# Kernel optimization log

Hardware: AMD Instinct MI355X
Metric: run time of the kernel (lower is better)

## Reference

```python
import jax, jax.numpy as jnp
import numpy as np

HOPS = 3  # max_hops; C has HOPS+1 embedding tables


def setup_inputs() -> dict:
    key = jax.random.key(0)
    k1, k2 = jax.random.split(key)
    # story: [memory_len, batch, token_size]
    story = jax.random.randint(k1, (2048, 64, 4), 0, 50000, dtype=jnp.int64)
    # stacked embedding tables C_0..C_3: [hop+1, vocab, embed_dim], N(0, 0.1)
    C = 0.1 * jax.random.normal(k2, (HOPS + 1, 50000, 128), dtype=jnp.float32)
    return {"story": story, "C": C}


def reference(story, C):
    # story: [M, B, T] -> [B, M, T]
    story = jnp.transpose(story, (1, 0, 2))
    B, M, T = story.shape
    D = C.shape[-1]
    # padding_idx=0 semantics: embedding of token 0 is zero (fwd and bwd)
    pad_mask = (story != 0).astype(C.dtype)[..., None]  # [B, M, T, 1]

    u = jnp.zeros((B, D), dtype=C.dtype)
    for hop in range(HOPS):
        # gather + mask + sum over token dim -> memory keys m_A: [B, M, D]
        m_A = jnp.sum(C[hop][story] * pad_mask, axis=2)
        # attention scores over memory slots, softmax along M
        prob = jax.nn.softmax(jnp.einsum('bmd,bd->bm', m_A, u), axis=1)
        # memory values m_C from next-hop table: [B, M, D]
        m_C = jnp.sum(C[hop + 1][story] * pad_mask, axis=2)
        o_k = jnp.einsum('bm,bmd->bd', prob, m_C)
        u = u + o_k
    return u
```

## Files before the change

kernel.cpp:

```cpp
#include <hip/hip_runtime.h>

#define MM 2048
#define BB 64
#define TT 4
#define DD 128
#define VV 50000
#define VPAD 50176
#define NPART 392

typedef float f4v __attribute__((ext_vector_type(4)));
typedef short s8v __attribute__((ext_vector_type(8)));

__device__ __forceinline__ unsigned short f2bf(float f) {
    unsigned int u = __float_as_uint(f);
    u = u + 0x7FFFu + ((u >> 16) & 1u);
    return (unsigned short)(u >> 16);
}

__global__ void k_init(float4* __restrict__ p) {
    p[blockIdx.x * 256 + threadIdx.x] = make_float4(0.f, 0.f, 0.f, 0.f);
}

__global__ __launch_bounds__(256) void k_scatter0(const int* __restrict__ st,
                                                  float* __restrict__ W) {
    const int g = blockIdx.x * 256 + threadIdx.x;
    const int b = g & 63;
    const float p = 1.0f / (float)MM;
    const int4 tk = *(const int4*)(st + (size_t)g * 4);
    if (tk.x) atomicAdd(W + (size_t)tk.x * 64 + b, p);
    if (tk.y) atomicAdd(W + (size_t)tk.y * 64 + b, p);
    if (tk.z) atomicAdd(W + (size_t)tk.z * 64 + b, p);
    if (tk.w) atomicAdd(W + (size_t)tk.w * 64 + b, p);
}

__global__ __launch_bounds__(256, 3) void k_gemm_p(const float* __restrict__ Ch,
                                                   const float* __restrict__ u,
                                                   float* __restrict__ P) {
    __shared__ short lds[192 * 136];
    const int t = threadIdx.x;
    const int v0 = blockIdx.x * 128;

#pragma unroll
    for (int i = 0; i < 24; ++i) {
        const int G = i * 256 + t;
        const int row = G >> 5;
        const int c4 = G & 31;
        float4 val;
        if (row < 128) {
            const int v = v0 + row;
            val = (v < VV) ? *(const float4*)(Ch + (size_t)v * DD + c4 * 4)
                           : make_float4(0.f, 0.f, 0.f, 0.f);
        } else {
            val = *(const float4*)(u + (size_t)(row - 128) * DD + c4 * 4);
        }
        const unsigned int lo = ((unsigned int)f2bf(val.y) << 16) | f2bf(val.x);
        const unsigned int hi = ((unsigned int)f2bf(val.w) << 16) | f2bf(val.z);
        *(uint2*)(lds + row * 136 + c4 * 4) = make_uint2(lo, hi);
    }
    __syncthreads();

    const int l = t & 63;
    const int w = t >> 6;
    const int quad = l >> 4;
    const int n16 = l & 15;

    const int ar0 = (32 * w + n16) * 136;
    const int ar1 = (32 * w + 16 + n16) * 136;
    const int br0 = (128 + n16) * 136;
    const int br1 = (144 + n16) * 136;
    const int br2 = (160 + n16) * 136;
    const int br3 = (176 + n16) * 136;

    f4v c00 = {0.f, 0.f, 0.f, 0.f}, c01 = c00, c02 = c00, c03 = c00;
    f4v c10 = c00, c11 = c00, c12 = c00, c13 = c00;

#pragma unroll
    for (int s = 0; s < 4; ++s) {
        const int ko = s * 32 + quad * 8;
        const s8v a0 = *(const s8v*)(lds + ar0 + ko);
        const s8v a1 = *(const s8v*)(lds + ar1 + ko);
        const s8v b0 = *(const s8v*)(lds + br0 + ko);
        const s8v b1 = *(const s8v*)(lds + br1 + ko);
        const s8v b2 = *(const s8v*)(lds + br2 + ko);
        const s8v b3 = *(const s8v*)(lds + br3 + ko);
        c00 = __builtin_amdgcn_mfma_f32_16x16x32_bf16(a0, b0, c00, 0, 0, 0);
        c01 = __builtin_amdgcn_mfma_f32_16x16x32_bf16(a0, b1, c01, 0, 0, 0);
        c02 = __builtin_amdgcn_mfma_f32_16x16x32_bf16(a0, b2, c02, 0, 0, 0);
        c03 = __builtin_amdgcn_mfma_f32_16x16x32_bf16(a0, b3, c03, 0, 0, 0);
        c10 = __builtin_amdgcn_mfma_f32_16x16x32_bf16(a1, b0, c10, 0, 0, 0);
        c11 = __builtin_amdgcn_mfma_f32_16x16x32_bf16(a1, b1, c11, 0, 0, 0);
        c12 = __builtin_amdgcn_mfma_f32_16x16x32_bf16(a1, b2, c12, 0, 0, 0);
        c13 = __builtin_amdgcn_mfma_f32_16x16x32_bf16(a1, b3, c13, 0, 0, 0);
    }

    const int vb0 = v0 + 32 * w + quad * 4;
    const int vb1 = vb0 + 16;
#pragma unroll
    for (int r = 0; r < 4; ++r) {
        float* __restrict__ P0 = P + (size_t)(vb0 + r) * 64 + n16;
        P0[0] = c00[r]; P0[16] = c01[r]; P0[32] = c02[r]; P0[48] = c03[r];
        float* __restrict__ P1 = P + (size_t)(vb1 + r) * 64 + n16;
        P1[0] = c10[r]; P1[16] = c11[r]; P1[32] = c12[r]; P1[48] = c13[r];
    }
}

__global__ __launch_bounds__(512) void k_attn(const int* __restrict__ st,
                                              const float* __restrict__ P,
                                              float* __restrict__ W) {
    const int b = blockIdx.x;
    const int tid = threadIdx.x;
    __shared__ float redsum[8];

    const int4 tk0 = *(const int4*)(st + ((size_t)(tid + 0)    * 64 + b) * 4);
    const int4 tk1 = *(const int4*)(st + ((size_t)(tid + 512)  * 64 + b) * 4);
    const int4 tk2 = *(const int4*)(st + ((size_t)(tid + 1024) * 64 + b) * 4);
    const int4 tk3 = *(const int4*)(st + ((size_t)(tid + 1536) * 64 + b) * 4);

    float v0 = 0.f, v1 = 0.f, v2 = 0.f, v3 = 0.f;
    if (tk0.x) v0 += P[(size_t)tk0.x * 64 + b];
    if (tk0.y) v0 += P[(size_t)tk0.y * 64 + b];
    if (tk0.z) v0 += P[(size_t)tk0.z * 64 + b];
    if (tk0.w) v0 += P[(size_t)tk0.w * 64 + b];
    if (tk1.x) v1 += P[(size_t)tk1.x * 64 + b];
    if (tk1.y) v1 += P[(size_t)tk1.y * 64 + b];
    if (tk1.z) v1 += P[(size_t)tk1.z * 64 + b];
    if (tk1.w) v1 += P[(size_t)tk1.w * 64 + b];
    if (tk2.x) v2 += P[(size_t)tk2.x * 64 + b];
    if (tk2.y) v2 += P[(size_t)tk2.y * 64 + b];
    if (tk2.z) v2 += P[(size_t)tk2.z * 64 + b];
    if (tk2.w) v2 += P[(size_t)tk2.w * 64 + b];
    if (tk3.x) v3 += P[(size_t)tk3.x * 64 + b];
    if (tk3.y) v3 += P[(size_t)tk3.y * 64 + b];
    if (tk3.z) v3 += P[(size_t)tk3.z * 64 + b];
    if (tk3.w) v3 += P[(size_t)tk3.w * 64 + b];

    v0 = __expf(v0); v1 = __expf(v1); v2 = __expf(v2); v3 = __expf(v3);
    float sum = (v0 + v1) + (v2 + v3);
#pragma unroll
    for (int off = 32; off; off >>= 1) sum += __shfl_xor(sum, off, 64);
    if ((tid & 63) == 0) redsum[tid >> 6] = sum;
    __syncthreads();
    float tot = redsum[0];
#pragma unroll
    for (int i = 1; i < 8; ++i) tot += redsum[i];
    const float inv = 1.f / tot;

    v0 *= inv; v1 *= inv; v2 *= inv; v3 *= inv;

    if (tk0.x) atomicAdd(W + (size_t)tk0.x * 64 + b, v0);
    if (tk0.y) atomicAdd(W + (size_t)tk0.y * 64 + b, v0);
    if (tk0.z) atomicAdd(W + (size_t)tk0.z * 64 + b, v0);
    if (tk0.w) atomicAdd(W + (size_t)tk0.w * 64 + b, v0);
    if (tk1.x) atomicAdd(W + (size_t)tk1.x * 64 + b, v1);
    if (tk1.y) atomicAdd(W + (size_t)tk1.y * 64 + b, v1);
    if (tk1.z) atomicAdd(W + (size_t)tk1.z * 64 + b, v1);
    if (tk1.w) atomicAdd(W + (size_t)tk1.w * 64 + b, v1);
    if (tk2.x) atomicAdd(W + (size_t)tk2.x * 64 + b, v2);
    if (tk2.y) atomicAdd(W + (size_t)tk2.y * 64 + b, v2);
    if (tk2.z) atomicAdd(W + (size_t)tk2.z * 64 + b, v2);
    if (tk2.w) atomicAdd(W + (size_t)tk2.w * 64 + b, v2);
    if (tk3.x) atomicAdd(W + (size_t)tk3.x * 64 + b, v3);
    if (tk3.y) atomicAdd(W + (size_t)tk3.y * 64 + b, v3);
    if (tk3.z) atomicAdd(W + (size_t)tk3.z * 64 + b, v3);
    if (tk3.w) atomicAdd(W + (size_t)tk3.w * 64 + b, v3);
}

__global__ __launch_bounds__(256, 3) void k_gemm_o(const float* __restrict__ C2,
                                                   float* __restrict__ W,
                                                   float* __restrict__ upart,
                                                   const int rezero) {
    __shared__ unsigned Wt[64 * 68];
    __shared__ unsigned Ct[128 * 68];
    const int t = threadIdx.x;
    const int vb = blockIdx.x * 128;

#pragma unroll
    for (int i = 0; i < 4; ++i) {
        const int item = i * 256 + t;
        const int q = item & 15;
        const int p = item >> 4;
        float* w0 = W + (size_t)(vb + 2 * p) * 64 + 4 * q;
        float* w1 = W + (size_t)(vb + 2 * p + 1) * 64 + 4 * q;
        const float4 x = *(const float4*)w0;
        const float4 y = *(const float4*)w1;
        if (rezero) {
            *(float4*)w0 = make_float4(0.f, 0.f, 0.f, 0.f);
            *(float4*)w1 = make_float4(0.f, 0.f, 0.f, 0.f);
        }
        Wt[(4 * q + 0) * 68 + p] = ((unsigned)f2bf(y.x) << 16) | f2bf(x.x);
        Wt[(4 * q + 1) * 68 + p] = ((unsigned)f2bf(y.y) << 16) | f2bf(x.y);
        Wt[(4 * q + 2) * 68 + p] = ((unsigned)f2bf(y.z) << 16) | f2bf(x.z);
        Wt[(4 * q + 3) * 68 + p] = ((unsigned)f2bf(y.w) << 16) | f2bf(x.w);
    }
#pragma unroll
    for (int i = 0; i < 8; ++i) {
        const int item = i * 256 + t;
        const int q = item & 31;
        const int p = item >> 5;
        const int v0 = vb + 2 * p;
        const float4 x = (v0 < VV)
            ? *(const float4*)(C2 + (size_t)v0 * DD + 4 * q)
            : make_float4(0.f, 0.f, 0.f, 0.f);
        const float4 y = (v0 + 1 < VV)
            ? *(const float4*)(C2 + (size_t)(v0 + 1) * DD + 4 * q)
            : make_float4(0.f, 0.f, 0.f, 0.f);
        Ct[(4 * q + 0) * 68 + p] = ((unsigned)f2bf(y.x) << 16) | f2bf(x.x);
        Ct[(4 * q + 1) * 68 + p] = ((unsigned)f2bf(y.y) << 16) | f2bf(x.y);
        Ct[(4 * q + 2) * 68 + p] = ((unsigned)f2bf(y.z) << 16) | f2bf(x.z);
        Ct[(4 * q + 3) * 68 + p] = ((unsigned)f2bf(y.w) << 16) | f2bf(x.w);
    }
    __syncthreads();

    const int l = t & 63;
    const int w = t >> 6;
    const int quad = l >> 4;
    const int n16 = l & 15;

    f4v a00 = {0.f, 0.f, 0.f, 0.f}, a01 = a00;
    f4v a10 = a00, a11 = a00, a20 = a00, a21 = a00, a30 = a00, a31 = a00;

#pragma unroll
    for (int ch = 0; ch < 4; ++ch) {
        const int ku = ch * 16 + quad * 4;
        const s8v wa0 = *(const s8v*)&Wt[(0  + n16) * 68 + ku];
        const s8v wa1 = *(const s8v*)&Wt[(16 + n16) * 68 + ku];
        const s8v wa2 = *(const s8v*)&Wt[(32 + n16) * 68 + ku];
        const s8v wa3 = *(const s8v*)&Wt[(48 + n16) * 68 + ku];
        const s8v cb0 = *(const s8v*)&Ct[(w * 32 + n16) * 68 + ku];
        const s8v cb1 = *(const s8v*)&Ct[(w * 32 + 16 + n16) * 68 + ku];
        a00 = __builtin_amdgcn_mfma_f32_16x16x32_bf16(wa0, cb0, a00, 0, 0, 0);
        a01 = __builtin_amdgcn_mfma_f32_16x16x32_bf16(wa0, cb1, a01, 0, 0, 0);
        a10 = __builtin_amdgcn_mfma_f32_16x16x32_bf16(wa1, cb0, a10, 0, 0, 0);
        a11 = __builtin_amdgcn_mfma_f32_16x16x32_bf16(wa1, cb1, a11, 0, 0, 0);
        a20 = __builtin_amdgcn_mfma_f32_16x16x32_bf16(wa2, cb0, a20, 0, 0, 0);
        a21 = __builtin_amdgcn_mfma_f32_16x16x32_bf16(wa2, cb1, a21, 0, 0, 0);
        a30 = __builtin_amdgcn_mfma_f32_16x16x32_bf16(wa3, cb0, a30, 0, 0, 0);
        a31 = __builtin_amdgcn_mfma_f32_16x16x32_bf16(wa3, cb1, a31, 0, 0, 0);
    }

    float* __restrict__ up = upart + (size_t)blockIdx.x * (BB * DD);
    const int dc = w * 32 + n16;
#pragma unroll
    for (int r = 0; r < 4; ++r) {
        const int br = quad * 4 + r;
        up[(br +  0) * DD + dc]      = a00[r];
        up[(br +  0) * DD + dc + 16] = a01[r];
        up[(br + 16) * DD + dc]      = a10[r];
        up[(br + 16) * DD + dc + 16] = a11[r];
        up[(br + 32) * DD + dc]      = a20[r];
        up[(br + 32) * DD + dc + 16] = a21[r];
        up[(br + 48) * DD + dc]      = a30[r];
        up[(br + 48) * DD + dc + 16] = a31[r];
    }
}

__global__ __launch_bounds__(256) void k_reduce_a(const float* __restrict__ up,
                                                  float* __restrict__ u) {
    const int jc = blockIdx.x & 31;
    const int kc = blockIdx.x >> 5;
    const int j = jc * 256 + threadIdx.x;
    const float* __restrict__ p = up + (size_t)kc * 49 * (BB * DD) + j;
    float s = 0.f;
#pragma unroll 7
    for (int k = 0; k < 49; ++k) s += p[(size_t)k * (BB * DD)];
    atomicAdd(u + j, s);
}

__global__ __launch_bounds__(256) void k_reduce_fin(const float* __restrict__ up,
                                                    const float* __restrict__ u,
                                                    float* __restrict__ out) {
    const int j = blockIdx.x * 256 + threadIdx.x;
    const float* __restrict__ p = up + j;
    float s = 0.f;
#pragma unroll 8
    for (int k = 0; k < NPART; ++k) s += p[(size_t)k * (BB * DD)];
    out[j] = u[j] + s;
}

extern "C" void kernel_launch(void* const* d_in, const int* in_sizes, int n_in,
                              void* d_out, int out_size, void* d_ws, size_t ws_size,
                              hipStream_t stream) {
    const int* st = (const int*)d_in[0];
    const float* C = (const float*)d_in[1];

    float* u  = (float*)d_ws;
    float* W  = u + BB * DD;
    float* P  = W + (size_t)VPAD * BB;
    float* up = P + (size_t)VPAD * BB;

    k_init<<<(BB * DD + VPAD * BB) / 1024, 256, 0, stream>>>((float4*)u);

    k_scatter0<<<(MM * BB) / 256, 256, 0, stream>>>(st, W);
    k_gemm_o<<<VPAD / 128, 256, 0, stream>>>(C + (size_t)1 * VV * DD, W, up, 1);
    k_reduce_a<<<256, 256, 0, stream>>>(up, u);

    k_gemm_p<<<VPAD / 128, 256, 0, stream>>>(C + (size_t)1 * VV * DD, u, P);
    k_attn<<<BB, 512, 0, stream>>>(st, P, W);
    k_gemm_o<<<VPAD / 128, 256, 0, stream>>>(C + (size_t)2 * VV * DD, W, up, 1);
    k_reduce_a<<<256, 256, 0, stream>>>(up, u);

    k_gemm_p<<<VPAD / 128, 256, 0, stream>>>(C + (size_t)2 * VV * DD, u, P);
    k_attn<<<BB, 512, 0, stream>>>(st, P, W);
    k_gemm_o<<<VPAD / 128, 256, 0, stream>>>(C + (size_t)3 * VV * DD, W, up, 0);
    k_reduce_fin<<<32, 256, 0, stream>>>(up, u, (float*)d_out);
}
```

Before: 326.9 us.

## Defer softmax normalization to reductions and spread attention across many blocks

The attention kernel is split from 64 blocks (one per batch) into 512 blocks over flattened memory-batch slots. It scatters unnormalized exp scores into W and writes per-block partial sums of the denominator. The normalization by 1/Z is moved into the later reduce kernels, which recompute Z from the partials. This removes the per-batch block-wide reduction barrier and the low block count, at the cost of extra partial-sum reads in the reduce kernels and no max subtraction, same as before.

```diff
diff --git a/kernel.cpp b/kernel.cpp
--- a/kernel.cpp
+++ b/kernel.cpp
@@ -7,6 +7,7 @@
 #define VV 50000
 #define VPAD 50176
 #define NPART 392
+#define NATT 512
 
 typedef float f4v __attribute__((ext_vector_type(4)));
 typedef short s8v __attribute__((ext_vector_type(8)));
@@ -104,65 +105,33 @@
     }
 }
 
-__global__ __launch_bounds__(512) void k_attn(const int* __restrict__ st,
-                                              const float* __restrict__ P,
-                                              float* __restrict__ W) {
-    const int b = blockIdx.x;
+__global__ __launch_bounds__(256) void k_attn2(const int* __restrict__ st,
+                                               const float* __restrict__ P,
+                                               float* __restrict__ W,
+                                               float* __restrict__ Zp) {
+    __shared__ float eb[256];
     const int tid = threadIdx.x;
-    __shared__ float redsum[8];
-
-    const int4 tk0 = *(const int4*)(st + ((size_t)(tid + 0)    * 64 + b) * 4);
-    const int4 tk1 = *(const int4*)(st + ((size_t)(tid + 512)  * 64 + b) * 4);
-    const int4 tk2 = *(const int4*)(st + ((size_t)(tid + 1024) * 64 + b) * 4);
-    const int4 tk3 = *(const int4*)(st + ((size_t)(tid + 1536) * 64 + b) * 4);
-
-    float v0 = 0.f, v1 = 0.f, v2 = 0.f, v3 = 0.f;
-    if (tk0.x) v0 += P[(size_t)tk0.x * 64 + b];
-    if (tk0.y) v0 += P[(size_t)tk0.y * 64 + b];
-    if (tk0.z) v0 += P[(size_t)tk0.z * 64 + b];
-    if (tk0.w) v0 += P[(size_t)tk0.w * 64 + b];
-    if (tk1.x) v1 += P[(size_t)tk1.x * 64 + b];
-    if (tk1.y) v1 += P[(size_t)tk1.y * 64 + b];
-    if (tk1.z) v1 += P[(size_t)tk1.z * 64 + b];
-    if (tk1.w) v1 += P[(size_t)tk1.w * 64 + b];
-    if (tk2.x) v2 += P[(size_t)tk2.x * 64 + b];
-    if (tk2.y) v2 += P[(size_t)tk2.y * 64 + b];
-    if (tk2.z) v2 += P[(size_t)tk2.z * 64 + b];
-    if (tk2.w) v2 += P[(size_t)tk2.w * 64 + b];
-    if (tk3.x) v3 += P[(size_t)tk3.x * 64 + b];
-    if (tk3.y) v3 += P[(size_t)tk3.y * 64 + b];
-    if (tk3.z) v3 += P[(size_t)tk3.z * 64 + b];
-    if (tk3.w) v3 += P[(size_t)tk3.w * 64 + b];
-
-    v0 = __expf(v0); v1 = __expf(v1); v2 = __expf(v2); v3 = __expf(v3);
-    float sum = (v0 + v1) + (v2 + v3);
-#pragma unroll
-    for (int off = 32; off; off >>= 1) sum += __shfl_xor(sum, off, 64);
-    if ((tid & 63) == 0) redsum[tid >> 6] = sum;
+    const int g = blockIdx.x * 256 + tid;
+    const int b = g & 63;
+
+    const int4 tk = *(const int4*)(st + (size_t)g * 4);
+    float s = 0.f;
+    if (tk.x) s += P[(size_t)tk.x * 64 + b];
+    if (tk.y) s += P[(size_t)tk.y * 64 + b];
+    if (tk.z) s += P[(size_t)tk.z * 64 + b];
+    if (tk.w) s += P[(size_t)tk.w * 64 + b];
+    const float e = __expf(s);
+    eb[tid] = e;
+
+    if (tk.x) atomicAdd(W + (size_t)tk.x * 64 + b, e);
+    if (tk.y) atomicAdd(W + (size_t)tk.y * 64 + b, e);
+    if (tk.z) atomicAdd(W + (size_t)tk.z * 64 + b, e);
+    if (tk.w) atomicAdd(W + (size_t)tk.w * 64 + b, e);
+
     __syncthreads();
-    float tot = redsum[0];
-#pragma unroll
-    for (int i = 1; i < 8; ++i) tot += redsum[i];
-    const float inv = 1.f / tot;
-
-    v0 *= inv; v1 *= inv; v2 *= inv; v3 *= inv;
-
-    if (tk0.x) atomicAdd(W + (size_t)tk0.x * 64 + b, v0);
-    if (tk0.y) atomicAdd(W + (size_t)tk0.y * 64 + b, v0);
-    if (tk0.z) atomicAdd(W + (size_t)tk0.z * 64 + b, v0);
-    if (tk0.w) atomicAdd(W + (size_t)tk0.w * 64 + b, v0);
-    if (tk1.x) atomicAdd(W + (size_t)tk1.x * 64 + b, v1);
-    if (tk1.y) atomicAdd(W + (size_t)tk1.y * 64 + b, v1);
-    if (tk1.z) atomicAdd(W + (size_t)tk1.z * 64 + b, v1);
-    if (tk1.w) atomicAdd(W + (size_t)tk1.w * 64 + b, v1);
-    if (tk2.x) atomicAdd(W + (size_t)tk2.x * 64 + b, v2);
-    if (tk2.y) atomicAdd(W + (size_t)tk2.y * 64 + b, v2);
-    if (tk2.z) atomicAdd(W + (size_t)tk2.z * 64 + b, v2);
-    if (tk2.w) atomicAdd(W + (size_t)tk2.w * 64 + b, v2);
-    if (tk3.x) atomicAdd(W + (size_t)tk3.x * 64 + b, v3);
-    if (tk3.y) atomicAdd(W + (size_t)tk3.y * 64 + b, v3);
-    if (tk3.z) atomicAdd(W + (size_t)tk3.z * 64 + b, v3);
-    if (tk3.w) atomicAdd(W + (size_t)tk3.w * 64 + b, v3);
+    if (tid < 64)
+        Zp[(size_t)blockIdx.x * 64 + tid] =
+            (eb[tid] + eb[tid + 64]) + (eb[tid + 128] + eb[tid + 192]);
 }
 
 __global__ __launch_bounds__(256, 3) void k_gemm_o(const float* __restrict__ C2,
@@ -254,6 +223,21 @@
     }
 }
 
+__device__ __forceinline__ float zfor(const float* __restrict__ Zp,
+                                      float* __restrict__ zw,
+                                      int b_base, int tid) {
+    const int bloc = tid >> 7;
+    const int b = b_base + bloc;
+    const int i = tid & 127;
+    float z = (Zp[(size_t)(i +   0) * 64 + b] + Zp[(size_t)(i + 128) * 64 + b])
+            + (Zp[(size_t)(i + 256) * 64 + b] + Zp[(size_t)(i + 384) * 64 + b]);
+#pragma unroll
+    for (int off = 32; off; off >>= 1) z += __shfl_xor(z, off, 64);
+    if ((tid & 63) == 0) zw[tid >> 6] = z;
+    __syncthreads();
+    return (bloc == 0) ? (zw[0] + zw[1]) : (zw[2] + zw[3]);
+}
+
 __global__ __launch_bounds__(256) void k_reduce_a(const float* __restrict__ up,
                                                   float* __restrict__ u) {
     const int jc = blockIdx.x & 31;
@@ -266,15 +250,37 @@
     atomicAdd(u + j, s);
 }
 
-__global__ __launch_bounds__(256) void k_reduce_fin(const float* __restrict__ up,
-                                                    const float* __restrict__ u,
-                                                    float* __restrict__ out) {
-    const int j = blockIdx.x * 256 + threadIdx.x;
+__global__ __launch_bounds__(256) void k_reduce_az(const float* __restrict__ up,
+                                                   const float* __restrict__ Zp,
+                                                   float* __restrict__ u) {
+    __shared__ float zw[4];
+    const int jc = blockIdx.x & 31;
+    const int kc = blockIdx.x >> 5;
+    const int tid = threadIdx.x;
+    const float Z = zfor(Zp, zw, jc * 2, tid);
+    const float rz = 1.f / Z;
+    const int j = jc * 256 + tid;
+    const float* __restrict__ p = up + (size_t)kc * 49 * (BB * DD) + j;
+    float s = 0.f;
+#pragma unroll 7
+    for (int k = 0; k < 49; ++k) s += p[(size_t)k * (BB * DD)];
+    atomicAdd(u + j, s * rz);
+}
+
+__global__ __launch_bounds__(256) void k_reduce_finz(const float* __restrict__ up,
+                                                     const float* __restrict__ Zp,
+                                                     const float* __restrict__ u,
+                                                     float* __restrict__ out) {
+    __shared__ float zw[4];
+    const int tid = threadIdx.x;
+    const float Z = zfor(Zp, zw, blockIdx.x * 2, tid);
+    const float rz = 1.f / Z;
+    const int j = blockIdx.x * 256 + tid;
     const float* __restrict__ p = up + j;
     float s = 0.f;
 #pragma unroll 8
     for (int k = 0; k < NPART; ++k) s += p[(size_t)k * (BB * DD)];
-    out[j] = u[j] + s;
+    out[j] = u[j] + s * rz;
 }
 
 extern "C" void kernel_launch(void* const* d_in, const int* in_sizes, int n_in,
@@ -287,6 +293,7 @@
     float* W  = u + BB * DD;
     float* P  = W + (size_t)VPAD * BB;
     float* up = P + (size_t)VPAD * BB;
+    float* Zp = up + (size_t)NPART * BB * DD;
 
     k_init<<<(BB * DD + VPAD * BB) / 1024, 256, 0, stream>>>((float4*)u);
 
@@ -295,12 +302,12 @@
     k_reduce_a<<<256, 256, 0, stream>>>(up, u);
 
     k_gemm_p<<<VPAD / 128, 256, 0, stream>>>(C + (size_t)1 * VV * DD, u, P);
-    k_attn<<<BB, 512, 0, stream>>>(st, P, W);
+    k_attn2<<<NATT, 256, 0, stream>>>(st, P, W, Zp);
     k_gemm_o<<<VPAD / 128, 256, 0, stream>>>(C + (size_t)2 * VV * DD, W, up, 1);
-    k_reduce_a<<<256, 256, 0, stream>>>(up, u);
+    k_reduce_az<<<256, 256, 0, stream>>>(up, Zp, u);
 
     k_gemm_p<<<VPAD / 128, 256, 0, stream>>>(C + (size_t)2 * VV * DD, u, P);
-    k_attn<<<BB, 512, 0, stream>>>(st, P, W);
+    k_attn2<<<NATT, 256, 0, stream>>>(st, P, W, Zp);
     k_gemm_o<<<VPAD / 128, 256, 0, stream>>>(C + (size_t)3 * VV * DD, W, up, 0);
-    k_reduce_fin<<<32, 256, 0, stream>>>(up, u, (float*)d_out);
-}
+    k_reduce_finz<<<32, 256, 0, stream>>>(up, Zp, u, (float*)d_out);
+}
```

Result: faster. 315.2 us (-3.6%).
